# Kernel tuning notes

Hardware: AMD Instinct MI355X
Metric: run time of the kernel (lower is better)

## Reference

```python
import jax, jax.numpy as jnp
import numpy as np

L = 512      # x_len (also per-segment memory length)
B = 4        # batch
D = 512      # d_model
H = 8        # num_head
DH = 64      # d_head
MEM = 3      # mem_num (number of cached memory segments)
TOTAL = (MEM + 1) * L
SCALE = 1.0 / (DH ** 0.5)
LN_EPS = 1e-5


def setup_inputs() -> dict:
    key = jax.random.key(0)
    ks = jax.random.split(key, 12)
    f = lambda k, s: jax.random.normal(k, s, dtype=jnp.float32)
    x = f(ks[0], (L, B, D))
    memory = f(ks[1], (MEM, L, B, D))
    pos_emb = f(ks[2], (TOTAL, B, D))
    pos_bias_u = f(ks[3], (H, DH)) * 0.02
    pos_bias_v = f(ks[4], (H, DH)) * 0.02
    # segment gate: random 0/1, but current-input segment (last) always on
    ib = (jax.random.uniform(ks[5], (L, B, MEM + 1)) < 0.7).astype(jnp.float32)
    indice_bool = ib.at[:, :, MEM].set(1.0)
    # causal mask over concatenated [memory ; x] keys: mask future input positions
    qi = jnp.arange(L)[:, None]
    kj = jnp.arange(TOTAL)[None, :]
    mask = jnp.broadcast_to((kj > (MEM * L + qi))[:, :, None], (L, TOTAL, B))
    W_q = f(ks[6], (D, H * DH)) * 0.02
    W_kv = f(ks[7], (D, 2 * H * DH)) * 0.02
    W_rel = f(ks[8], (D, H * DH)) * 0.02
    W_o = f(ks[9], (H * DH, D)) * 0.02
    ln_g = jnp.ones((D,), jnp.float32)
    ln_b = jnp.zeros((D,), jnp.float32)
    return dict(x=x, memory=memory, pos_emb=pos_emb, pos_bias_u=pos_bias_u,
                pos_bias_v=pos_bias_v, mask=mask, indice_bool=indice_bool,
                W_q=W_q, W_kv=W_kv, W_rel=W_rel, W_o=W_o, ln_g=ln_g, ln_b=ln_b)


def _rel_shift(bd):
    # bd: [i, k, j, b, n]; torch _rel_shift flattens (k,j) and does the pad/view trick
    i, k, j, b, n = bd.shape
    xf = bd.reshape(i, k * j, b, n)
    zp = jnp.zeros((i, 1, b, n), bd.dtype)
    xp = jnp.concatenate([zp, xf], axis=1)            # [i, k*j+1, b, n]
    xp = xp.reshape(k * j + 1, i, b, n)               # raw memory reinterpretation
    return xp[1:].reshape(i, k, j, b, n)


def reference(x, memory, pos_emb, pos_bias_u, pos_bias_v, mask, indice_bool,
              W_q, W_kv, W_rel, W_o, ln_g, ln_b):
    Lq, Bz, Dm = x.shape
    mem_flat = memory.reshape(MEM * Lq, Bz, Dm)
    c = jnp.concatenate([mem_flat, x], axis=0)        # [TOTAL, B, D]
    kv = c @ W_kv                                     # [TOTAL, B, 2*H*DH]
    k_, v_ = jnp.split(kv, 2, axis=-1)
    pk = k_.reshape(MEM + 1, Lq, Bz, H, DH)
    pv = v_.reshape(MEM + 1, Lq, Bz, H, DH)
    rel = (pos_emb @ W_rel).reshape(MEM + 1, Lq, Bz, H, DH)
    q = (x @ W_q).reshape(Lq, Bz, H, DH)
    qu = q + pos_bias_u
    qv = q + pos_bias_v
    # gate[i,k,1,b,1] == indice_bool[i,b,k]; equals einsum('ibnd,ibk->kibnd') pre-mul
    gate = jnp.transpose(indice_bool, (0, 2, 1))[:, :, None, :, None]
    AC = jnp.einsum('ibnd,kjbnd->ikjbn', qu, pk) * gate   # [i,k,j,b,n]
    BD = jnp.einsum('ibnd,kjbnd->ikjbn', qv, rel) * gate
    BD = _rel_shift(BD)
    score = (AC + BD) * SCALE
    score = score.reshape(Lq, TOTAL, Bz, H)
    score = jnp.where(mask[:, :, :, None], -jnp.inf, score)
    prob = jax.nn.softmax(score, axis=1)
    attn_matrix = prob.mean(axis=(2, 3))              # [i, TOTAL]
    prob5 = prob.reshape(Lq, MEM + 1, Lq, Bz, H)
    vec = jnp.einsum('ikjbn,kjbnd->ibnd', prob5, pv).reshape(Lq, Bz, H * DH)
    attn_out = vec @ W_o
    y = x + attn_out
    mu = y.mean(-1, keepdims=True)
    var = jnp.mean(jnp.square(y - mu), axis=-1, keepdims=True)
    output = (y - mu) / jnp.sqrt(var + LN_EPS) * ln_g + ln_b
    return (output, attn_matrix)
```

## Files before the change

### kernel.cpp

```cpp
#include <hip/hip_runtime.h>
#include <hip/hip_bf16.h>
#include <math.h>

typedef __bf16 bhalf8 __attribute__((ext_vector_type(8)));
typedef __bf16 bhalf4 __attribute__((ext_vector_type(4)));
typedef float  f32x4  __attribute__((ext_vector_type(4)));

#define MFMA16(a, b, c) __builtin_amdgcn_mfma_f32_16x16x32_bf16(a, b, c, 0, 0, 0)

__global__ __launch_bounds__(256) void cast_bf16(const float* __restrict__ in,
                                                 __bf16* __restrict__ out, int n4)
{
  const int i = blockIdx.x * 256 + threadIdx.x;
  if (i < n4) {
    float4 v = ((const float4*)in)[i];
    bhalf4 o;
    o[0] = (__bf16)v.x; o[1] = (__bf16)v.y; o[2] = (__bf16)v.z; o[3] = (__bf16)v.w;
    ((bhalf4*)out)[i] = o;
  }
}

__global__ __launch_bounds__(256) void transcast(const float* __restrict__ W,
                                                 __bf16* __restrict__ Wt, int K, int N)
{
  const int k = blockIdx.x * 64 + (threadIdx.x & 63);
  const int n = blockIdx.y * 4 + (threadIdx.x >> 6);
  Wt[(size_t)n * K + k] = (__bf16)W[(size_t)k * N + n];
}

template <int OUT_F32>
__global__ __launch_bounds__(256) void gemm_bf16(
    const __bf16* __restrict__ A, const __bf16* __restrict__ Bt,
    void* __restrict__ C, int M, int N, int K)
{
  __shared__ __bf16 a_lds[128][40];
  __shared__ __bf16 b_lds[128][40];
  const int m0 = blockIdx.x * 128;
  const int n0 = blockIdx.y * 128;
  const int tid = threadIdx.x;
  const int w = tid >> 6, l = tid & 63;
  const int wn = (w >> 1) * 64, wm = (w & 1) * 64;
  const int li = l & 15, lq = l >> 4;
  const int lk = lq << 3;

  f32x4 acc[4][4] = {};

  for (int k0 = 0; k0 < K; k0 += 32) {
    __syncthreads();
#pragma unroll
    for (int c = 0; c < 2; ++c) {
      const int chunk = c * 256 + tid;
      const int row = chunk >> 2, kc = (chunk & 3) << 3;
      *(bhalf8*)&a_lds[row][kc] = *(const bhalf8*)(A + (size_t)(m0 + row) * K + k0 + kc);
      *(bhalf8*)&b_lds[row][kc] = *(const bhalf8*)(Bt + (size_t)(n0 + row) * K + k0 + kc);
    }
    __syncthreads();
    bhalf8 af[4], bf_[4];
#pragma unroll
    for (int s = 0; s < 4; ++s) {
      af[s]  = *(const bhalf8*)&b_lds[wn + s * 16 + li][lk];
      bf_[s] = *(const bhalf8*)&a_lds[wm + s * 16 + li][lk];
    }
#pragma unroll
    for (int ns = 0; ns < 4; ++ns)
#pragma unroll
      for (int ms = 0; ms < 4; ++ms)
        acc[ns][ms] = MFMA16(af[ns], bf_[ms], acc[ns][ms]);
  }

  const int lr = lq << 2;
#pragma unroll
  for (int ms = 0; ms < 4; ++ms) {
    const int m = m0 + wm + ms * 16 + li;
#pragma unroll
    for (int ns = 0; ns < 4; ++ns) {
      const int n = n0 + wn + ns * 16 + lr;
      if (OUT_F32) {
        *(f32x4*)((float*)C + (size_t)m * N + n) = acc[ns][ms];
      } else {
        bhalf4 pk;
#pragma unroll
        for (int r = 0; r < 4; ++r) pk[r] = (__bf16)acc[ns][ms][r];
        *(bhalf4*)((__bf16*)C + (size_t)m * N + n) = pk;
      }
    }
  }
}

__global__ __launch_bounds__(256) void vtrans(const __bf16* __restrict__ kvb,
                                              __bf16* __restrict__ vtb)
{
  __shared__ __bf16 T2[64][72];
  const int t0 = blockIdx.x * 64;
  const int p = blockIdx.y;
  const int b = p >> 3, n = p & 7;
  const int tid = threadIdx.x;
#pragma unroll
  for (int c = 0; c < 2; ++c) {
    const int e = c * 256 + tid;
    const int tl = e >> 3, d8 = (e & 7) << 3;
    bhalf8 v8 = *(const bhalf8*)(kvb + ((size_t)(t0 + tl) * 4 + b) * 1024 + 512 + n * 64 + d8);
#pragma unroll
    for (int j = 0; j < 8; ++j) T2[d8 + j][tl] = v8[j];
  }
  __syncthreads();
#pragma unroll
  for (int c = 0; c < 2; ++c) {
    const int e = c * 256 + tid;
    const int d = e >> 3, t8 = (e & 7) << 3;
    bhalf8 v = *(const bhalf8*)&T2[d][t8];
    *(bhalf8*)(vtb + ((size_t)p * 64 + d) * 2048 + t0 + t8) = v;
  }
}

__global__ __launch_bounds__(512, 4) void attn_v3(
    const __bf16* __restrict__ qb_, const __bf16* __restrict__ kvb,
    const __bf16* __restrict__ relb, const __bf16* __restrict__ vtb,
    const float* __restrict__ pbu, const float* __restrict__ pbv,
    const float* __restrict__ indice,
    __bf16* __restrict__ vecb, float* __restrict__ ml)
{
  __shared__ __align__(16) __bf16 P_l[32][136];
  __shared__ __align__(16) __bf16 bdl[160][33];
  __shared__ float red0[8][33];
  __shared__ float red1[8][33];
  __shared__ float lfin[32];

  const int bid = blockIdx.x;
  const int wrk = ((bid & 7) << 6) + (bid >> 3);
  const int plane = wrk >> 4;
  const int i0 = (wrk & 15) << 5;
  const int b = plane >> 3, n = plane & 7;
  const int tid = threadIdx.x;
  const int w = tid >> 6;
  const int l = tid & 63;
  const int li = l & 15;
  const int lq = l >> 4;

  const __bf16* kbase = kvb + (size_t)b * 1024 + n * 64;
  const __bf16* rbase = relb + (size_t)b * 512 + n * 64;
  const __bf16* vbase = vtb + (size_t)plane * 131072;

  bhalf8 qu[2][2], qv[2][2];
  float g[2][4];
#pragma unroll
  for (int it = 0; it < 2; ++it) {
    const int i = i0 + it * 16 + li;
    const float* gp = indice + ((size_t)i * 4 + b) * 4;
    g[it][0] = gp[0]; g[it][1] = gp[1]; g[it][2] = gp[2]; g[it][3] = gp[3];
#pragma unroll
    for (int h = 0; h < 2; ++h) {
      const int dc = h * 32 + lq * 8;
      bhalf8 q8 = *(const bhalf8*)(qb_ + ((size_t)i * 4 + b) * 512 + n * 64 + dc);
      float ub[8], vb[8];
      *(float4*)&ub[0] = *(const float4*)(pbu + n * 64 + dc);
      *(float4*)&ub[4] = *(const float4*)(pbu + n * 64 + dc + 4);
      *(float4*)&vb[0] = *(const float4*)(pbv + n * 64 + dc);
      *(float4*)&vb[4] = *(const float4*)(pbv + n * 64 + dc + 4);
      bhalf8 a, c;
#pragma unroll
      for (int j = 0; j < 8; ++j) {
        const float qf = (float)q8[j];
        a[j] = (__bf16)(qf + ub[j]);
        c[j] = (__bf16)(qf + vb[j]);
      }
      qu[it][h] = a; qv[it][h] = c;
    }
  }

  float m0 = -1e30f, m1 = -1e30f, l0 = 0.f, l1 = 0.f;
  f32x4 oacc = {0.f, 0.f, 0.f, 0.f};
  const int dgw = w >> 1, itw = w & 1;
  const int nt = ((1536 + i0 + 31) >> 7) + 1;

  for (int tile = 0; tile < nt; ++tile) {
    const int tb = tile << 7;
    const int rb = tb + 480 - i0;

#pragma unroll
    for (int ri = 0; ri < 2; ++ri) {
      const int rs = w + ri * 8;
      if (ri == 0 || rs < 10) {
        int row = rb + rs * 16 + li;
        row = row > 2047 ? 2047 : row;
        const __bf16* rp = rbase + (size_t)row * 2048;
        bhalf8 a0 = *(const bhalf8*)(rp + lq * 8);
        bhalf8 a1 = *(const bhalf8*)(rp + 32 + lq * 8);
#pragma unroll
        for (int it = 0; it < 2; ++it) {
          f32x4 c = {0.f, 0.f, 0.f, 0.f};
          c = MFMA16(a0, qv[it][0], c);
          c = MFMA16(a1, qv[it][1], c);
#pragma unroll
          for (int r = 0; r < 4; ++r) {
            const int rowl = rs * 16 + lq * 4 + r;
            int rk = (rb + rowl) >> 9; rk = rk > 3 ? 3 : rk;
            bdl[rowl][it * 16 + li] = (__bf16)(c[r] * g[it][rk]);
          }
        }
      }
    }
    f32x4 s[2];
    {
      const __bf16* kp = kbase + (size_t)(tb + w * 16 + li) * 4096;
      bhalf8 a0 = *(const bhalf8*)(kp + lq * 8);
      bhalf8 a1 = *(const bhalf8*)(kp + 32 + lq * 8);
#pragma unroll
      for (int it = 0; it < 2; ++it) {
        f32x4 c = {0.f, 0.f, 0.f, 0.f};
        c = MFMA16(a0, qu[it][0], c);
        c = MFMA16(a1, qu[it][1], c);
        s[it] = c;
      }
    }
    __syncthreads();

    float sv[2][4];
    float tmax[2] = {-1e30f, -1e30f};
#pragma unroll
    for (int it = 0; it < 2; ++it) {
      const int i = i0 + it * 16 + li;
#pragma unroll
      for (int r = 0; r < 4; ++r) {
        const int tl = w * 16 + lq * 4 + r;
        const int t = tb + tl;
        float sc = -1e30f;
        if (t <= 1536 + i) {
          const float bdv = (float)bdl[tl + 31 - it * 16 - li][it * 16 + li];
          sc = (s[it][r] * g[it][t >> 9] + bdv) * 0.125f;
        }
        sv[it][r] = sc;
        tmax[it] = fmaxf(tmax[it], sc);
      }
    }
    tmax[0] = fmaxf(tmax[0], __shfl_xor(tmax[0], 16));
    tmax[0] = fmaxf(tmax[0], __shfl_xor(tmax[0], 32));
    tmax[1] = fmaxf(tmax[1], __shfl_xor(tmax[1], 16));
    tmax[1] = fmaxf(tmax[1], __shfl_xor(tmax[1], 32));
    if (l < 16) { red0[w][li] = tmax[0]; red0[w][16 + li] = tmax[1]; }
    __syncthreads();

    float mn[2], scl[2];
#pragma unroll
    for (int it = 0; it < 2; ++it) {
      const int ic = it * 16 + li;
      float mt = red0[0][ic];
#pragma unroll
      for (int ww = 1; ww < 8; ++ww) mt = fmaxf(mt, red0[ww][ic]);
      const float mo = it ? m1 : m0;
      mn[it] = fmaxf(mo, mt);
      scl[it] = __expf(mo - mn[it]);
    }
    float ps[2] = {0.f, 0.f};
#pragma unroll
    for (int it = 0; it < 2; ++it) {
      bhalf4 pk;
#pragma unroll
      for (int r = 0; r < 4; ++r) {
        const float p = __expf(sv[it][r] - mn[it]);
        ps[it] += p;
        pk[r] = (__bf16)p;
      }
      *(bhalf4*)&P_l[it * 16 + li][w * 16 + lq * 4] = pk;
    }
    ps[0] += __shfl_xor(ps[0], 16); ps[0] += __shfl_xor(ps[0], 32);
    ps[1] += __shfl_xor(ps[1], 16); ps[1] += __shfl_xor(ps[1], 32);
    if (l < 16) { red1[w][li] = ps[0]; red1[w][16 + li] = ps[1]; }
    __syncthreads();

    {
      float ls0 = 0.f, ls1 = 0.f;
#pragma unroll
      for (int ww = 0; ww < 8; ++ww) { ls0 += red1[ww][li]; ls1 += red1[ww][16 + li]; }
      l0 = l0 * scl[0] + ls0; m0 = mn[0];
      l1 = l1 * scl[1] + ls1; m1 = mn[1];
    }
    oacc *= scl[itw];
    {
      const __bf16* vp = vbase + (size_t)(dgw * 16 + li) * 2048 + tb;
#pragma unroll
      for (int kt = 0; kt < 4; ++kt) {
        bhalf8 af = *(const bhalf8*)(vp + kt * 32 + lq * 8);
        bhalf8 bf_ = *(const bhalf8*)&P_l[itw * 16 + li][kt * 32 + lq * 8];
        oacc = MFMA16(af, bf_, oacc);
      }
    }
  }

  __syncthreads();
  float* obuf = (float*)&P_l[0][0];
  if (w == 0 && l < 16) {
    lfin[li] = 1.f / l0;
    lfin[16 + li] = 1.f / l1;
    float* mp0 = ml + ((size_t)plane * 512 + i0 + li) * 2;
    mp0[0] = m0; mp0[1] = l0;
    float* mp1 = ml + ((size_t)plane * 512 + i0 + 16 + li) * 2;
    mp1[0] = m1; mp1[1] = l1;
  }
#pragma unroll
  for (int r = 0; r < 4; ++r)
    obuf[(itw * 16 + li) * 68 + dgw * 16 + lq * 4 + r] = oacc[r];
  __syncthreads();
  {
    const int iloc = tid >> 4, dq = tid & 15;
    const float rli = lfin[iloc];
    f32x4 o = *(f32x4*)&obuf[iloc * 68 + dq * 4];
    bhalf4 ov;
#pragma unroll
    for (int r = 0; r < 4; ++r) ov[r] = (__bf16)(o[r] * rli);
    *(bhalf4*)(vecb + ((size_t)(i0 + iloc) * 4 + b) * 512 + n * 64 + dq * 4) = ov;
  }
}

__global__ __launch_bounds__(512, 4) void am_v3(
    const __bf16* __restrict__ qb_, const __bf16* __restrict__ kvb,
    const __bf16* __restrict__ relb, const float* __restrict__ pbu,
    const float* __restrict__ pbv, const float* __restrict__ indice,
    const float* __restrict__ ml, float* __restrict__ am_p)
{
  __shared__ __align__(16) __bf16 bdl[160][33];
  __shared__ __align__(16) float Lt[32][132];

  const int bid = blockIdx.x;
  const int wrk = ((bid & 7) << 7) + (bid >> 3);
  const int bx = wrk & 15;
  const int by = (wrk >> 4) & 15;
  const int b  = wrk >> 8;
  const int tb = bx << 7, i0 = by << 5;
  const int tid = threadIdx.x;
  const int w = tid >> 6;
  const int l = tid & 63;
  const int li = l & 15;
  const int lq = l >> 4;

  float* outb = am_p + (size_t)b * 1048576;

  if (tb > 1536 + i0 + 31) {
#pragma unroll
    for (int c = 0; c < 2; ++c) {
      const int e = c * 512 + tid;
      const int iloc = e >> 5, tq = e & 31;
      f32x4 z = {0.f, 0.f, 0.f, 0.f};
      *(f32x4*)(outb + (size_t)(i0 + iloc) * 2048 + tb + tq * 4) = z;
    }
    return;
  }
  const int rb = tb + 480 - i0;
  float acc[2][4] = {};

  for (int nn = 0; nn < 8; ++nn) {
    const int plane = b * 8 + nn;
    const __bf16* kbase = kvb + (size_t)b * 1024 + nn * 64;
    const __bf16* rbase = relb + (size_t)b * 512 + nn * 64;
    bhalf8 qu[2][2], qv[2][2];
    float g[2][4], mrow[2], rl[2];
#pragma unroll
    for (int it = 0; it < 2; ++it) {
      const int i = i0 + it * 16 + li;
      const float* gp = indice + ((size_t)i * 4 + b) * 4;
      g[it][0] = gp[0]; g[it][1] = gp[1]; g[it][2] = gp[2]; g[it][3] = gp[3];
      const float* mp = ml + ((size_t)plane * 512 + i) * 2;
      mrow[it] = mp[0]; rl[it] = 1.f / mp[1];
#pragma unroll
      for (int h = 0; h < 2; ++h) {
        const int dc = h * 32 + lq * 8;
        bhalf8 q8 = *(const bhalf8*)(qb_ + ((size_t)i * 4 + b) * 512 + nn * 64 + dc);
        float ub[8], vb[8];
        *(float4*)&ub[0] = *(const float4*)(pbu + nn * 64 + dc);
        *(float4*)&ub[4] = *(const float4*)(pbu + nn * 64 + dc + 4);
        *(float4*)&vb[0] = *(const float4*)(pbv + nn * 64 + dc);
        *(float4*)&vb[4] = *(const float4*)(pbv + nn * 64 + dc + 4);
        bhalf8 a, c;
#pragma unroll
        for (int j = 0; j < 8; ++j) {
          const float qf = (float)q8[j];
          a[j] = (__bf16)(qf + ub[j]);
          c[j] = (__bf16)(qf + vb[j]);
        }
        qu[it][h] = a; qv[it][h] = c;
      }
    }
#pragma unroll
    for (int ri = 0; ri < 2; ++ri) {
      const int rs = w + ri * 8;
      if (ri == 0 || rs < 10) {
        int row = rb + rs * 16 + li;
        row = row > 2047 ? 2047 : row;
        const __bf16* rp = rbase + (size_t)row * 2048;
        bhalf8 a0 = *(const bhalf8*)(rp + lq * 8);
        bhalf8 a1 = *(const bhalf8*)(rp + 32 + lq * 8);
#pragma unroll
        for (int it = 0; it < 2; ++it) {
          f32x4 c = {0.f, 0.f, 0.f, 0.f};
          c = MFMA16(a0, qv[it][0], c);
          c = MFMA16(a1, qv[it][1], c);
#pragma unroll
          for (int r = 0; r < 4; ++r) {
            const int rowl = rs * 16 + lq * 4 + r;
            int rk = (rb + rowl) >> 9; rk = rk > 3 ? 3 : rk;
            bdl[rowl][it * 16 + li] = (__bf16)(c[r] * g[it][rk]);
          }
        }
      }
    }
    f32x4 s[2];
    {
      const __bf16* kp = kbase + (size_t)(tb + w * 16 + li) * 4096;
      bhalf8 a0 = *(const bhalf8*)(kp + lq * 8);
      bhalf8 a1 = *(const bhalf8*)(kp + 32 + lq * 8);
#pragma unroll
      for (int it = 0; it < 2; ++it) {
        f32x4 c = {0.f, 0.f, 0.f, 0.f};
        c = MFMA16(a0, qu[it][0], c);
        c = MFMA16(a1, qu[it][1], c);
        s[it] = c;
      }
    }
    __syncthreads();
#pragma unroll
    for (int it = 0; it < 2; ++it) {
      const int i = i0 + it * 16 + li;
#pragma unroll
      for (int r = 0; r < 4; ++r) {
        const int tl = w * 16 + lq * 4 + r;
        const int t = tb + tl;
        if (t <= 1536 + i) {
          const float bdv = (float)bdl[tl + 31 - it * 16 - li][it * 16 + li];
          const float sc = (s[it][r] * g[it][t >> 9] + bdv) * 0.125f;
          acc[it][r] += __expf(sc - mrow[it]) * rl[it];
        }
      }
    }
    __syncthreads();
  }
#pragma unroll
  for (int it = 0; it < 2; ++it)
#pragma unroll
    for (int r = 0; r < 4; ++r)
      Lt[it * 16 + li][w * 16 + lq * 4 + r] = acc[it][r] * 0.03125f;
  __syncthreads();
#pragma unroll
  for (int c = 0; c < 2; ++c) {
    const int e = c * 512 + tid;
    const int iloc = e >> 5, tq = e & 31;
    f32x4 v = *(f32x4*)&Lt[iloc][tq * 4];
    *(f32x4*)(outb + (size_t)(i0 + iloc) * 2048 + tb + tq * 4) = v;
  }
}

__global__ __launch_bounds__(256) void am_reduce(const float* __restrict__ am_p,
                                                 float* __restrict__ am)
{
  const size_t i = ((size_t)blockIdx.x * 256 + threadIdx.x) * 4;
  f32x4 v = *(const f32x4*)(am_p + i);
  v += *(const f32x4*)(am_p + 1048576 + i);
  v += *(const f32x4*)(am_p + 2097152 + i);
  v += *(const f32x4*)(am_p + 3145728 + i);
  *(f32x4*)(am + i) = v;
}

__global__ __launch_bounds__(256) void ln_f32(
    const float* __restrict__ x, const float* __restrict__ ao,
    const float* __restrict__ g, const float* __restrict__ bb,
    float* __restrict__ out)
{
  const int row = blockIdx.x;
  const int tid = threadIdx.x;
  const size_t base = (size_t)row * 512;
  const float y0 = x[base + tid] + ao[base + tid];
  const float y1 = x[base + 256 + tid] + ao[base + 256 + tid];
  float s  = y0 + y1;
  float ss = y0 * y0 + y1 * y1;
#pragma unroll
  for (int off = 32; off > 0; off >>= 1) {
    s  += __shfl_xor(s, off);
    ss += __shfl_xor(ss, off);
  }
  __shared__ float sred[4], ssred[4], stat[2];
  const int w = tid >> 6;
  if ((tid & 63) == 0) { sred[w] = s; ssred[w] = ss; }
  __syncthreads();
  if (tid == 0) {
    const float S  = sred[0] + sred[1] + sred[2] + sred[3];
    const float SS = ssred[0] + ssred[1] + ssred[2] + ssred[3];
    const float mu = S * (1.f / 512.f);
    const float var = SS * (1.f / 512.f) - mu * mu;
    stat[0] = mu;
    stat[1] = rsqrtf(var + 1e-5f);
  }
  __syncthreads();
  const float mu = stat[0], rs = stat[1];
  out[base + tid]       = (y0 - mu) * rs * g[tid] + bb[tid];
  out[base + 256 + tid] = (y1 - mu) * rs * g[256 + tid] + bb[256 + tid];
}

extern "C" void kernel_launch(void* const* d_in, const int* in_sizes, int n_in,
                              void* d_out, int out_size, void* d_ws, size_t ws_size,
                              hipStream_t stream)
{
  (void)in_sizes; (void)n_in; (void)out_size; (void)ws_size;
  const float* x      = (const float*)d_in[0];
  const float* memory = (const float*)d_in[1];
  const float* pos    = (const float*)d_in[2];
  const float* pbu    = (const float*)d_in[3];
  const float* pbv    = (const float*)d_in[4];
  const float* indice = (const float*)d_in[6];
  const float* W_q    = (const float*)d_in[7];
  const float* W_kv   = (const float*)d_in[8];
  const float* W_rel  = (const float*)d_in[9];
  const float* W_o    = (const float*)d_in[10];
  const float* ln_g   = (const float*)d_in[11];
  const float* ln_b   = (const float*)d_in[12];

  float* out = (float*)d_out;
  float* am  = out + 1048576;

  __bf16* cb    = (__bf16*)d_ws;
  __bf16* posb  = cb + 4194304;
  __bf16* qb    = posb + 4194304;
  __bf16* kvb   = qb + 1048576;
  __bf16* relb  = kvb + 8388608;
  __bf16* vecb  = relb + 4194304;
  __bf16* wqt   = vecb + 1048576;
  __bf16* wkvt  = wqt + 262144;
  __bf16* wrelt = wkvt + 524288;
  __bf16* wot   = wrelt + 262144;
  float*  aof   = (float*)(wot + 262144);
  float*  ml    = aof + 1048576;
  __bf16* xb    = cb + 3145728;
  __bf16* vtb   = cb;
  float*  am_p  = (float*)d_ws;

  cast_bf16<<<3072, 256, 0, stream>>>(memory, cb, 786432);
  cast_bf16<<<1024, 256, 0, stream>>>(x, xb, 262144);
  cast_bf16<<<4096, 256, 0, stream>>>(pos, posb, 1048576);
  transcast<<<dim3(8, 128), 256, 0, stream>>>(W_q,   wqt,   512, 512);
  transcast<<<dim3(8, 256), 256, 0, stream>>>(W_kv,  wkvt,  512, 1024);
  transcast<<<dim3(8, 128), 256, 0, stream>>>(W_rel, wrelt, 512, 512);
  transcast<<<dim3(8, 128), 256, 0, stream>>>(W_o,   wot,   512, 512);

  gemm_bf16<0><<<dim3(16, 4), 256, 0, stream>>>(xb,   wqt,  qb,  2048, 512, 512);
  gemm_bf16<0><<<dim3(64, 8), 256, 0, stream>>>(cb,   wkvt, kvb, 8192, 1024, 512);
  gemm_bf16<0><<<dim3(64, 4), 256, 0, stream>>>(posb, wrelt, relb, 8192, 512, 512);

  vtrans<<<dim3(32, 32), 256, 0, stream>>>(kvb, vtb);

  attn_v3<<<512, 512, 0, stream>>>(qb, kvb, relb, vtb, pbu, pbv, indice, vecb, ml);

  am_v3<<<1024, 512, 0, stream>>>(qb, kvb, relb, pbu, pbv, indice, ml, am_p);
  am_reduce<<<1024, 256, 0, stream>>>(am_p, am);

  gemm_bf16<1><<<dim3(16, 4), 256, 0, stream>>>(vecb, wot, aof, 2048, 512, 512);
  ln_f32<<<2048, 256, 0, stream>>>(x, aof, ln_g, ln_b, out);
}
```

Measured before the change: 369.8 us.

## Fuse position biases and scale into Q GEMM epilogue; restructure attention-map kernel per head

The Q projection GEMM now adds pos_bias_u/v and the 1/sqrt(d) scale in its epilogue. It writes two head-major bf16 tensors (qu, qv), so both attention kernels load Q directly instead of recomputing biased Q per block. The attention-map kernel is rewritten so that each warp handles one head for a 16-row by 128-key tile, and per-head probabilities are summed with LDS atomics. This replaces the old sequential loop over 8 heads with its repeated syncthreads. Folding the scale into bf16 Q slightly changes rounding, and the LDS atomics may contend.

```diff
diff --git a/kernel.cpp b/kernel.cpp
--- a/kernel.cpp
+++ b/kernel.cpp
@@ -28,10 +28,12 @@
   Wt[(size_t)n * K + k] = (__bf16)W[(size_t)k * N + n];
 }
 
-template <int OUT_F32>
+template <int OUT_MODE>
 __global__ __launch_bounds__(256) void gemm_bf16(
     const __bf16* __restrict__ A, const __bf16* __restrict__ Bt,
-    void* __restrict__ C, int M, int N, int K)
+    void* __restrict__ C, int M, int N, int K,
+    const float* __restrict__ pbu, const float* __restrict__ pbv,
+    __bf16* __restrict__ qup, __bf16* __restrict__ qvp)
 {
   __shared__ __bf16 a_lds[128][40];
   __shared__ __bf16 b_lds[128][40];
@@ -75,13 +77,29 @@
 #pragma unroll
     for (int ns = 0; ns < 4; ++ns) {
       const int n = n0 + wn + ns * 16 + lr;
-      if (OUT_F32) {
+      if (OUT_MODE == 1) {
         *(f32x4*)((float*)C + (size_t)m * N + n) = acc[ns][ms];
-      } else {
+      } else if (OUT_MODE == 0) {
         bhalf4 pk;
 #pragma unroll
         for (int r = 0; r < 4; ++r) pk[r] = (__bf16)acc[ns][ms][r];
         *(bhalf4*)((__bf16*)C + (size_t)m * N + n) = pk;
+      } else {
+        const int i = m >> 2, bb = m & 3, hd = n >> 6;
+        float4 u4 = *(const float4*)(pbu + n);
+        float4 v4 = *(const float4*)(pbv + n);
+        const size_t off = (((size_t)bb * 8 + hd) * 512 + i) * 64 + (n & 63);
+        bhalf4 pu, pv;
+        pu[0] = (__bf16)((acc[ns][ms][0] + u4.x) * 0.125f);
+        pu[1] = (__bf16)((acc[ns][ms][1] + u4.y) * 0.125f);
+        pu[2] = (__bf16)((acc[ns][ms][2] + u4.z) * 0.125f);
+        pu[3] = (__bf16)((acc[ns][ms][3] + u4.w) * 0.125f);
+        pv[0] = (__bf16)((acc[ns][ms][0] + v4.x) * 0.125f);
+        pv[1] = (__bf16)((acc[ns][ms][1] + v4.y) * 0.125f);
+        pv[2] = (__bf16)((acc[ns][ms][2] + v4.z) * 0.125f);
+        pv[3] = (__bf16)((acc[ns][ms][3] + v4.w) * 0.125f);
+        *(bhalf4*)(qup + off) = pu;
+        *(bhalf4*)(qvp + off) = pv;
       }
     }
   }
@@ -114,10 +132,9 @@
 }
 
 __global__ __launch_bounds__(512, 4) void attn_v3(
-    const __bf16* __restrict__ qb_, const __bf16* __restrict__ kvb,
-    const __bf16* __restrict__ relb, const __bf16* __restrict__ vtb,
-    const float* __restrict__ pbu, const float* __restrict__ pbv,
-    const float* __restrict__ indice,
+    const __bf16* __restrict__ qup, const __bf16* __restrict__ qvp,
+    const __bf16* __restrict__ kvb, const __bf16* __restrict__ relb,
+    const __bf16* __restrict__ vtb, const float* __restrict__ indice,
     __bf16* __restrict__ vecb, float* __restrict__ ml)
 {
   __shared__ __align__(16) __bf16 P_l[32][136];
@@ -148,24 +165,12 @@
     const int i = i0 + it * 16 + li;
     const float* gp = indice + ((size_t)i * 4 + b) * 4;
     g[it][0] = gp[0]; g[it][1] = gp[1]; g[it][2] = gp[2]; g[it][3] = gp[3];
-#pragma unroll
-    for (int h = 0; h < 2; ++h) {
-      const int dc = h * 32 + lq * 8;
-      bhalf8 q8 = *(const bhalf8*)(qb_ + ((size_t)i * 4 + b) * 512 + n * 64 + dc);
-      float ub[8], vb[8];
-      *(float4*)&ub[0] = *(const float4*)(pbu + n * 64 + dc);
-      *(float4*)&ub[4] = *(const float4*)(pbu + n * 64 + dc + 4);
-      *(float4*)&vb[0] = *(const float4*)(pbv + n * 64 + dc);
-      *(float4*)&vb[4] = *(const float4*)(pbv + n * 64 + dc + 4);
-      bhalf8 a, c;
-#pragma unroll
-      for (int j = 0; j < 8; ++j) {
-        const float qf = (float)q8[j];
-        a[j] = (__bf16)(qf + ub[j]);
-        c[j] = (__bf16)(qf + vb[j]);
-      }
-      qu[it][h] = a; qv[it][h] = c;
-    }
+    const __bf16* qp = qup + ((size_t)plane * 512 + i) * 64;
+    const __bf16* qq = qvp + ((size_t)plane * 512 + i) * 64;
+    qu[it][0] = *(const bhalf8*)(qp + lq * 8);
+    qu[it][1] = *(const bhalf8*)(qp + 32 + lq * 8);
+    qv[it][0] = *(const bhalf8*)(qq + lq * 8);
+    qv[it][1] = *(const bhalf8*)(qq + 32 + lq * 8);
   }
 
   float m0 = -1e30f, m1 = -1e30f, l0 = 0.f, l1 = 0.f;
@@ -227,7 +232,7 @@
         float sc = -1e30f;
         if (t <= 1536 + i) {
           const float bdv = (float)bdl[tl + 31 - it * 16 - li][it * 16 + li];
-          sc = (s[it][r] * g[it][t >> 9] + bdv) * 0.125f;
+          sc = s[it][r] * g[it][t >> 9] + bdv;
         }
         sv[it][r] = sc;
         tmax[it] = fmaxf(tmax[it], sc);
@@ -312,139 +317,98 @@
   }
 }
 
-__global__ __launch_bounds__(512, 4) void am_v3(
-    const __bf16* __restrict__ qb_, const __bf16* __restrict__ kvb,
-    const __bf16* __restrict__ relb, const float* __restrict__ pbu,
-    const float* __restrict__ pbv, const float* __restrict__ indice,
-    const float* __restrict__ ml, float* __restrict__ am_p)
-{
-  __shared__ __align__(16) __bf16 bdl[160][33];
-  __shared__ __align__(16) float Lt[32][132];
+__global__ __launch_bounds__(512, 4) void am_v4(
+    const __bf16* __restrict__ qup, const __bf16* __restrict__ qvp,
+    const __bf16* __restrict__ kvb, const __bf16* __restrict__ relb,
+    const float* __restrict__ indice, const float* __restrict__ ml,
+    float* __restrict__ am_p)
+{
+  __shared__ __bf16 bdl[8][144][19];
+  __shared__ float accum[16][133];
 
   const int bid = blockIdx.x;
-  const int wrk = ((bid & 7) << 7) + (bid >> 3);
+  const int wrk = ((bid & 7) << 8) + (bid >> 3);
+  const int b  = wrk >> 9;
+  const int iy = (wrk >> 4) & 31;
   const int bx = wrk & 15;
-  const int by = (wrk >> 4) & 15;
-  const int b  = wrk >> 8;
-  const int tb = bx << 7, i0 = by << 5;
+  const int tb = bx << 7, i0 = iy << 4;
   const int tid = threadIdx.x;
-  const int w = tid >> 6;
-  const int l = tid & 63;
-  const int li = l & 15;
-  const int lq = l >> 4;
-
+  const int w = tid >> 6, l = tid & 63;
+  const int li = l & 15, lq = l >> 4;
   float* outb = am_p + (size_t)b * 1048576;
 
-  if (tb > 1536 + i0 + 31) {
-#pragma unroll
-    for (int c = 0; c < 2; ++c) {
-      const int e = c * 512 + tid;
-      const int iloc = e >> 5, tq = e & 31;
-      f32x4 z = {0.f, 0.f, 0.f, 0.f};
-      *(f32x4*)(outb + (size_t)(i0 + iloc) * 2048 + tb + tq * 4) = z;
+  if (tb > 1536 + i0 + 15) {
+#pragma unroll
+    for (int c = 0; c < 4; ++c) {
+      const int e = (c << 9) + tid;
+      const int iloc = e >> 7, tl = e & 127;
+      outb[(size_t)(i0 + iloc) * 2048 + tb + tl] = 0.f;
     }
     return;
   }
-  const int rb = tb + 480 - i0;
-  float acc[2][4] = {};
-
-  for (int nn = 0; nn < 8; ++nn) {
-    const int plane = b * 8 + nn;
-    const __bf16* kbase = kvb + (size_t)b * 1024 + nn * 64;
-    const __bf16* rbase = relb + (size_t)b * 512 + nn * 64;
-    bhalf8 qu[2][2], qv[2][2];
-    float g[2][4], mrow[2], rl[2];
-#pragma unroll
-    for (int it = 0; it < 2; ++it) {
-      const int i = i0 + it * 16 + li;
-      const float* gp = indice + ((size_t)i * 4 + b) * 4;
-      g[it][0] = gp[0]; g[it][1] = gp[1]; g[it][2] = gp[2]; g[it][3] = gp[3];
-      const float* mp = ml + ((size_t)plane * 512 + i) * 2;
-      mrow[it] = mp[0]; rl[it] = 1.f / mp[1];
-#pragma unroll
-      for (int h = 0; h < 2; ++h) {
-        const int dc = h * 32 + lq * 8;
-        bhalf8 q8 = *(const bhalf8*)(qb_ + ((size_t)i * 4 + b) * 512 + nn * 64 + dc);
-        float ub[8], vb[8];
-        *(float4*)&ub[0] = *(const float4*)(pbu + nn * 64 + dc);
-        *(float4*)&ub[4] = *(const float4*)(pbu + nn * 64 + dc + 4);
-        *(float4*)&vb[0] = *(const float4*)(pbv + nn * 64 + dc);
-        *(float4*)&vb[4] = *(const float4*)(pbv + nn * 64 + dc + 4);
-        bhalf8 a, c;
-#pragma unroll
-        for (int j = 0; j < 8; ++j) {
-          const float qf = (float)q8[j];
-          a[j] = (__bf16)(qf + ub[j]);
-          c[j] = (__bf16)(qf + vb[j]);
-        }
-        qu[it][h] = a; qv[it][h] = c;
-      }
-    }
-#pragma unroll
-    for (int ri = 0; ri < 2; ++ri) {
-      const int rs = w + ri * 8;
-      if (ri == 0 || rs < 10) {
-        int row = rb + rs * 16 + li;
-        row = row > 2047 ? 2047 : row;
-        const __bf16* rp = rbase + (size_t)row * 2048;
-        bhalf8 a0 = *(const bhalf8*)(rp + lq * 8);
-        bhalf8 a1 = *(const bhalf8*)(rp + 32 + lq * 8);
-#pragma unroll
-        for (int it = 0; it < 2; ++it) {
-          f32x4 c = {0.f, 0.f, 0.f, 0.f};
-          c = MFMA16(a0, qv[it][0], c);
-          c = MFMA16(a1, qv[it][1], c);
-#pragma unroll
-          for (int r = 0; r < 4; ++r) {
-            const int rowl = rs * 16 + lq * 4 + r;
-            int rk = (rb + rowl) >> 9; rk = rk > 3 ? 3 : rk;
-            bdl[rowl][it * 16 + li] = (__bf16)(c[r] * g[it][rk]);
-          }
-        }
-      }
-    }
-    f32x4 s[2];
-    {
-      const __bf16* kp = kbase + (size_t)(tb + w * 16 + li) * 4096;
-      bhalf8 a0 = *(const bhalf8*)(kp + lq * 8);
-      bhalf8 a1 = *(const bhalf8*)(kp + 32 + lq * 8);
-#pragma unroll
-      for (int it = 0; it < 2; ++it) {
-        f32x4 c = {0.f, 0.f, 0.f, 0.f};
-        c = MFMA16(a0, qu[it][0], c);
-        c = MFMA16(a1, qu[it][1], c);
-        s[it] = c;
-      }
-    }
-    __syncthreads();
-#pragma unroll
-    for (int it = 0; it < 2; ++it) {
-      const int i = i0 + it * 16 + li;
-#pragma unroll
-      for (int r = 0; r < 4; ++r) {
-        const int tl = w * 16 + lq * 4 + r;
-        const int t = tb + tl;
-        if (t <= 1536 + i) {
-          const float bdv = (float)bdl[tl + 31 - it * 16 - li][it * 16 + li];
-          const float sc = (s[it][r] * g[it][t >> 9] + bdv) * 0.125f;
-          acc[it][r] += __expf(sc - mrow[it]) * rl[it];
-        }
-      }
-    }
-    __syncthreads();
-  }
-#pragma unroll
-  for (int it = 0; it < 2; ++it)
-#pragma unroll
-    for (int r = 0; r < 4; ++r)
-      Lt[it * 16 + li][w * 16 + lq * 4 + r] = acc[it][r] * 0.03125f;
-  __syncthreads();
-#pragma unroll
-  for (int c = 0; c < 2; ++c) {
-    const int e = c * 512 + tid;
-    const int iloc = e >> 5, tq = e & 31;
-    f32x4 v = *(f32x4*)&Lt[iloc][tq * 4];
-    *(f32x4*)(outb + (size_t)(i0 + iloc) * 2048 + tb + tq * 4) = v;
+
+  const int rb = tb + 496 - i0;
+  const int p = b * 8 + w;
+
+  for (int f = tid; f < 2128; f += 512) ((float*)accum)[f] = 0.f;
+
+  const __bf16* qpp = qup + ((size_t)p * 512 + i0 + li) * 64;
+  const __bf16* qvv = qvp + ((size_t)p * 512 + i0 + li) * 64;
+  bhalf8 qu0 = *(const bhalf8*)(qpp + lq * 8);
+  bhalf8 qu1 = *(const bhalf8*)(qpp + 32 + lq * 8);
+  bhalf8 qv0 = *(const bhalf8*)(qvv + lq * 8);
+  bhalf8 qv1 = *(const bhalf8*)(qvv + 32 + lq * 8);
+  const float* gp = indice + ((size_t)(i0 + li) * 4 + b) * 4;
+  const float g0 = gp[0], g1 = gp[1], g2 = gp[2], g3 = gp[3];
+  const float* mp = ml + ((size_t)p * 512 + i0 + li) * 2;
+  const float mrow = mp[0];
+  const float rl = 1.f / mp[1];
+  __syncthreads();
+
+#pragma unroll
+  for (int rs = 0; rs < 9; ++rs) {
+    int row = rb + (rs << 4) + li;
+    row = row > 2047 ? 2047 : row;
+    const __bf16* rp = relb + ((size_t)row * 4 + b) * 512 + (w << 6);
+    bhalf8 a0 = *(const bhalf8*)(rp + lq * 8);
+    bhalf8 a1 = *(const bhalf8*)(rp + 32 + lq * 8);
+    f32x4 c = {0.f, 0.f, 0.f, 0.f};
+    c = MFMA16(a0, qv0, c);
+    c = MFMA16(a1, qv1, c);
+#pragma unroll
+    for (int r = 0; r < 4; ++r) {
+      const int rrow = (rs << 4) + (lq << 2) + r;
+      int rk = (rb + rrow) >> 9; rk = rk > 3 ? 3 : rk;
+      const float gk = rk == 0 ? g0 : (rk == 1 ? g1 : (rk == 2 ? g2 : g3));
+      bdl[w][rrow][li] = (__bf16)(c[r] * gk);
+    }
+  }
+#pragma unroll
+  for (int ts = 0; ts < 8; ++ts) {
+    const __bf16* kp = kvb + ((size_t)(tb + (ts << 4) + li) * 4 + b) * 1024 + (w << 6);
+    bhalf8 a0 = *(const bhalf8*)(kp + lq * 8);
+    bhalf8 a1 = *(const bhalf8*)(kp + 32 + lq * 8);
+    f32x4 s = {0.f, 0.f, 0.f, 0.f};
+    s = MFMA16(a0, qu0, s);
+    s = MFMA16(a1, qu1, s);
+#pragma unroll
+    for (int r = 0; r < 4; ++r) {
+      const int tl = (ts << 4) + (lq << 2) + r;
+      const int t = tb + tl;
+      if (t <= 1536 + i0 + li) {
+        const float bdv = (float)bdl[w][tl + 15 - li][li];
+        const float gk = (t >> 9) == 0 ? g0 : ((t >> 9) == 1 ? g1 : ((t >> 9) == 2 ? g2 : g3));
+        const float sc = s[r] * gk + bdv;
+        atomicAdd(&accum[li][tl], __expf(sc - mrow) * rl);
+      }
+    }
+  }
+  __syncthreads();
+#pragma unroll
+  for (int c = 0; c < 4; ++c) {
+    const int e = (c << 9) + tid;
+    const int iloc = e >> 7, tl = e & 127;
+    outb[(size_t)(i0 + iloc) * 2048 + tb + tl] = accum[iloc][tl] * 0.03125f;
   }
 }
 
@@ -517,19 +481,20 @@
 
   __bf16* cb    = (__bf16*)d_ws;
   __bf16* posb  = cb + 4194304;
-  __bf16* qb    = posb + 4194304;
-  __bf16* kvb   = qb + 1048576;
+  __bf16* kvb   = posb + 4194304;
   __bf16* relb  = kvb + 8388608;
-  __bf16* vecb  = relb + 4194304;
+  __bf16* qup   = relb + 4194304;
+  __bf16* qvp   = qup + 1048576;
+  __bf16* vecb  = qvp + 1048576;
   __bf16* wqt   = vecb + 1048576;
   __bf16* wkvt  = wqt + 262144;
   __bf16* wrelt = wkvt + 524288;
   __bf16* wot   = wrelt + 262144;
-  float*  aof   = (float*)(wot + 262144);
-  float*  ml    = aof + 1048576;
+  float*  ml    = (float*)(wot + 262144);
   __bf16* xb    = cb + 3145728;
   __bf16* vtb   = cb;
   float*  am_p  = (float*)d_ws;
+  float*  aof   = (float*)d_ws;
 
   cast_bf16<<<3072, 256, 0, stream>>>(memory, cb, 786432);
   cast_bf16<<<1024, 256, 0, stream>>>(x, xb, 262144);
@@ -539,17 +504,21 @@
   transcast<<<dim3(8, 128), 256, 0, stream>>>(W_rel, wrelt, 512, 512);
   transcast<<<dim3(8, 128), 256, 0, stream>>>(W_o,   wot,   512, 512);
 
-  gemm_bf16<0><<<dim3(16, 4), 256, 0, stream>>>(xb,   wqt,  qb,  2048, 512, 512);
-  gemm_bf16<0><<<dim3(64, 8), 256, 0, stream>>>(cb,   wkvt, kvb, 8192, 1024, 512);
-  gemm_bf16<0><<<dim3(64, 4), 256, 0, stream>>>(posb, wrelt, relb, 8192, 512, 512);
+  gemm_bf16<2><<<dim3(16, 4), 256, 0, stream>>>(xb, wqt, (void*)qup, 2048, 512, 512,
+                                                pbu, pbv, qup, qvp);
+  gemm_bf16<0><<<dim3(64, 8), 256, 0, stream>>>(cb, wkvt, kvb, 8192, 1024, 512,
+                                                nullptr, nullptr, nullptr, nullptr);
+  gemm_bf16<0><<<dim3(64, 4), 256, 0, stream>>>(posb, wrelt, relb, 8192, 512, 512,
+                                                nullptr, nullptr, nullptr, nullptr);
 
   vtrans<<<dim3(32, 32), 256, 0, stream>>>(kvb, vtb);
 
-  attn_v3<<<512, 512, 0, stream>>>(qb, kvb, relb, vtb, pbu, pbv, indice, vecb, ml);
-
-  am_v3<<<1024, 512, 0, stream>>>(qb, kvb, relb, pbu, pbv, indice, ml, am_p);
+  attn_v3<<<512, 512, 0, stream>>>(qup, qvp, kvb, relb, vtb, indice, vecb, ml);
+
+  am_v4<<<2048, 512, 0, stream>>>(qup, qvp, kvb, relb, indice, ml, am_p);
   am_reduce<<<1024, 256, 0, stream>>>(am_p, am);
 
-  gemm_bf16<1><<<dim3(16, 4), 256, 0, stream>>>(vecb, wot, aof, 2048, 512, 512);
+  gemm_bf16<1><<<dim3(16, 4), 256, 0, stream>>>(vecb, wot, aof, 2048, 512, 512,
+                                                nullptr, nullptr, nullptr, nullptr);
   ln_f32<<<2048, 256, 0, stream>>>(x, aof, ln_g, ln_b, out);
 }
```

Result: slower. 468.8 us (+26.8%).
